# Performance work log

Hardware: AMD Instinct MI355X
Metric: run time of the kernel (lower is better)

## Reference

```python
import jax, jax.numpy as jnp
import numpy as np

B, N, M, D = 8, 4096, 4096, 128


def _cdist(x, y):
    # Euclidean distance via gram trick (matches torch.cdist p=2 math)
    # x: (B,N,D), y: (B,M,D) -> (B,N,M)
    x2 = jnp.sum(x * x, axis=-1)  # (B,N)
    y2 = jnp.sum(y * y, axis=-1)  # (B,M)
    xy = jnp.einsum('bnd,bmd->bnm', x, y)  # (B,N,M)
    sq = x2[:, :, None] + y2[:, None, :] - 2.0 * xy
    return jnp.sqrt(jnp.maximum(sq, 0.0))


def setup_inputs() -> dict:
    key = jax.random.key(0)
    k1, k2 = jax.random.split(key)
    predicted_set = jax.random.normal(k1, (B, N, D), dtype=jnp.float32)
    target_set = jax.random.normal(k2, (B, M, D), dtype=jnp.float32)
    return {"predicted_set": predicted_set, "target_set": target_set}


def reference(predicted_set, target_set):
    pairwise = _cdist(predicted_set, target_set)       # (B,N,M)
    forward_distance = jnp.min(pairwise, axis=1)        # (B,M)  (min over predicted points)
    backward_distance = jnp.min(pairwise, axis=0)       # (N,M)  (min over BATCH, as in original code)
    # reduction = 'mean'
    return jnp.mean(forward_distance) + jnp.mean(backward_distance)
```

## Files before the change

### kernel.cpp

```cpp
#include <hip/hip_runtime.h>
#include <hip/hip_fp8.h>

#define BB 8
#define NN 4096
#define MM 4096
#define DD 128

typedef float f32x4  __attribute__((ext_vector_type(4)));
typedef float f32x16 __attribute__((ext_vector_type(16)));
typedef int   i32x4  __attribute__((ext_vector_type(4)));
typedef int   i32x8  __attribute__((ext_vector_type(8)));


typedef const __attribute__((address_space(1))) unsigned int* gas_ptr;
typedef __attribute__((address_space(3))) unsigned int* las_ptr;
static __device__ __forceinline__ void gload_lds16(const unsigned char* g,
                                                   unsigned char* l) {
    __builtin_amdgcn_global_load_lds((gas_ptr)g, (las_ptr)l, 16, 0, 0);
}

#define ISSUE_X(dst, addr)                                                  \
    asm volatile("global_load_dwordx4 %0, %4, off\n\t"                      \
                 "global_load_dwordx4 %1, %4, off offset:16\n\t"            \
                 "global_load_dwordx4 %2, %4, off offset:2048\n\t"          \
                 "global_load_dwordx4 %3, %4, off offset:2064"              \
                 : "=&v"(dst[0]), "=&v"(dst[1]), "=&v"(dst[2]), "=&v"(dst[3]) \
                 : "v"(addr))

#define WAIT_X(buf, N)                                                      \
    do {                                                                    \
        asm volatile("s_waitcnt vmcnt(" #N ")"                              \
                     : "+v"(buf[0]), "+v"(buf[1]), "+v"(buf[2]), "+v"(buf[3])); \
        __builtin_amdgcn_sched_barrier(0);                                  \
    } while (0)

__global__ __launch_bounds__(256)
void prep_all(const float* __restrict__ x, const float* __restrict__ y,
              unsigned char* __restrict__ xq, unsigned char* __restrict__ yq,
              float* __restrict__ x2, float* __restrict__ y2,
              unsigned int* __restrict__ fwd, float* __restrict__ bsum,
              float* __restrict__ fsum, unsigned int* __restrict__ counter) {
    __shared__ i32x4 lbuf[256];

    const int tid  = threadIdx.x;
    const int g    = blockIdx.x;
    const int gtid = g * 256 + tid;
    if (gtid < BB * MM) fwd[gtid] = 0x7f800000u;
    if (gtid == 0) { *bsum = 0.0f; *fsum = 0.0f; *counter = 0u; }

    const int rl = tid >> 3;
    const int c  = tid & 7;

    const float* src;
    unsigned char* dst;
    float* sq;
    float sgn;
    int row;
    if (g < 1024) {
        src = x; dst = xq + (size_t)g * 4096; sq = x2; sgn = 1.0f;
        row = g * 32 + rl;
    } else {
        src = y; dst = yq + (size_t)(g - 1024) * 4096; sq = y2; sgn = -1.0f;
        row = (g - 1024) * 32 + rl;
    }

    const f32x4* base = (const f32x4*)(src + (size_t)row * DD + c * 16);
    f32x4 v[4];
    #pragma unroll
    for (int j = 0; j < 4; ++j) v[j] = base[j];

    float s = 0.0f;
    #pragma unroll
    for (int j = 0; j < 4; ++j)
        s += v[j].x * v[j].x + v[j].y * v[j].y + v[j].z * v[j].z + v[j].w * v[j].w;

    i32x4 d;
    #pragma unroll
    for (int j = 0; j < 4; ++j) {
        unsigned int dj = (unsigned int)__builtin_amdgcn_cvt_pk_fp8_f32(
            sgn * v[j].x, sgn * v[j].y, 0, false);
        dj = (unsigned int)__builtin_amdgcn_cvt_pk_fp8_f32(
            sgn * v[j].z, sgn * v[j].w, (int)dj, true);
        d[j] = (int)dj;
    }

    const int lds_off = (c >> 2) * 2048 + ((c >> 1) & 1) * 1024
                      + rl * 32 + (c & 1) * 16;
    *(i32x4*)((char*)lbuf + lds_off) = d;

    #pragma unroll
    for (int m = 4; m; m >>= 1) s += __shfl_xor(s, m, 64);
    if (c == 0) sq[row] = 0.5f * s;

    __syncthreads();
    *(i32x4*)(dst + (size_t)tid * 16) = lbuf[tid];
}

__global__ __launch_bounds__(256, 4)
void chamfer_main(const unsigned char* __restrict__ xq, const unsigned char* __restrict__ yq,
                  const float* __restrict__ x2, const float* __restrict__ y2,
                  unsigned int* __restrict__ fwd, float* __restrict__ bpart) {
    __shared__ float x2s[BB][128];
    __shared__ float y2s[BB][32];
    __shared__ unsigned int fbuf[BB][32];
    __shared__ unsigned char ybuf[BB][4096];
    __shared__ float red[4];

    const int tid   = threadIdx.x;
    const int lane  = tid & 63;
    const int wave  = tid >> 6;
    const int lhalf = lane >> 5;
    const int l31   = lane & 31;

    const int id  = blockIdx.x;
    const int xcd = id & 7;
    const int j   = id >> 3;
    const int nb  = (xcd >> 1) * 8 + (j & 7);
    const int mb  = (xcd & 1) * 64 + (j >> 3);
    const int n0b = nb * 128;
    const int n0w = n0b + wave * 32;
    const int m0  = mb * 32;

    const size_t laneoff = (size_t)lhalf * 1024 + (size_t)l31 * 32;
    const unsigned char* xbase = xq + (size_t)(n0w >> 5) * 4096 + laneoff;

    const size_t ysw = (size_t)(wave >> 1) * 2048 + (size_t)(wave & 1) * 1024
                     + ((size_t)lhalf << 4) + (size_t)l31 * 32;
    const unsigned char* ybase = yq + (size_t)mb * 4096 + ysw;

    #pragma unroll
    for (int b = 0; b < BB; ++b)
        gload_lds16(ybase + ((size_t)b << 19), &ybuf[b][wave * 1024]);

    i32x4 fxr[2][4];
    ISSUE_X(fxr[0], xbase);

    for (int i = tid; i < BB * 128; i += 256)
        x2s[i >> 7][i & 127] = x2[(size_t)(i >> 7) * NN + n0b + (i & 127)];
    {
        int i = tid;
        y2s[i >> 5][i & 31] = y2[(size_t)(i >> 5) * MM + m0 + (i & 31)];
        ((unsigned int*)fbuf)[i] = 0x7f800000u;
    }
    __syncthreads();

    const float INF = __builtin_inff();
    float bmin[16];
    #pragma unroll
    for (int r = 0; r < 16; ++r) bmin[r] = INF;

    const int rb0 = lhalf * 1024 + l31 * 16;

    #pragma unroll
    for (int b = 0; b < BB; ++b) {
        const int cur = b & 1;
        if (b < BB - 1)
            ISSUE_X(fxr[cur ^ 1], (xbase + ((size_t)(b + 1) << 19)));

        if (b < BB - 1) { WAIT_X(fxr[cur], 4); }
        else            { WAIT_X(fxr[cur], 0); }

        float y2v = y2s[b][l31];
        f32x16 acc;
        #pragma unroll
        for (int q = 0; q < 4; ++q) {
            f32x4 xv = *(const f32x4*)&x2s[b][wave * 32 + lhalf * 4 + q * 8];
            #pragma unroll
            for (int e = 0; e < 4; ++e)
                acc[q * 4 + e] = xv[e] + y2v;
        }

        #pragma unroll
        for (int i = 0; i < 2; ++i) {
            i32x8 av = __builtin_shufflevector(fxr[cur][2 * i], fxr[cur][2 * i + 1],
                                               0, 1, 2, 3, 4, 5, 6, 7);
            const unsigned char* yb = &ybuf[b][i * 2048 + rb0];
            i32x4 lo = *(const i32x4*)(yb);
            i32x4 hi = *(const i32x4*)(yb + 512);
            i32x8 bv = __builtin_shufflevector(lo, hi, 0, 1, 2, 3, 4, 5, 6, 7);
            acc = __builtin_amdgcn_mfma_scale_f32_32x32x64_f8f6f4(
                av, bv, acc, 0, 0, 0, 127, 0, 127);
        }

        float fm = INF;
        #pragma unroll
        for (int r = 0; r < 16; ++r) {
            bmin[r] = fminf(bmin[r], acc[r]);
            fm      = fminf(fm, acc[r]);
        }
        atomicMin(&fbuf[b][l31], __float_as_uint(fmaxf(fm, 0.0f)));
    }
    __syncthreads();

    {
        int i = tid;
        atomicMin(&fwd[(size_t)(i >> 5) * MM + m0 + (i & 31)], fbuf[i >> 5][i & 31]);
    }

    float s = 0.0f;
    #pragma unroll
    for (int r = 0; r < 16; ++r)
        s += sqrtf(2.0f * fmaxf(bmin[r], 0.0f));
    #pragma unroll
    for (int off = 32; off; off >>= 1) s += __shfl_down(s, off, 64);
    if (lane == 0) red[wave] = s;
    __syncthreads();
    if (tid == 0) bpart[id] = red[0] + red[1] + red[2] + red[3];
}

__global__ __launch_bounds__(256)
void finalize_kernel(const unsigned int* __restrict__ fwd,
                     const float* __restrict__ bpart,
                     float* __restrict__ bsum, float* __restrict__ fsum,
                     unsigned int* __restrict__ counter, float* __restrict__ out) {
    __shared__ float redf[4], redb[4];
    __shared__ int isLast;
    const int tid = threadIdx.x, lane = tid & 63, wave = tid >> 6;
    const int gtid = blockIdx.x * 256 + tid;
    uint4 u = ((const uint4*)fwd)[gtid];
    float sf = sqrtf(2.0f * __uint_as_float(u.x)) + sqrtf(2.0f * __uint_as_float(u.y)) +
               sqrtf(2.0f * __uint_as_float(u.z)) + sqrtf(2.0f * __uint_as_float(u.w));
    float sb = (gtid < 4096) ? bpart[gtid] : 0.0f;
    #pragma unroll
    for (int off = 32; off; off >>= 1) {
        sf += __shfl_down(sf, off, 64);
        sb += __shfl_down(sb, off, 64);
    }
    if (lane == 0) { redf[wave] = sf; redb[wave] = sb; }
    __syncthreads();
    if (tid == 0) {
        atomicAdd(fsum, redf[0] + redf[1] + redf[2] + redf[3]);
        atomicAdd(bsum, redb[0] + redb[1] + redb[2] + redb[3]);
        __threadfence();
        unsigned int c = atomicAdd(counter, 1u);
        isLast = (c == gridDim.x - 1) ? 1 : 0;
        if (isLast) {
            __threadfence();
            float fs = __hip_atomic_load(fsum, __ATOMIC_RELAXED,
                                         __HIP_MEMORY_SCOPE_AGENT);
            float bs = __hip_atomic_load(bsum, __ATOMIC_RELAXED,
                                         __HIP_MEMORY_SCOPE_AGENT);
            out[0] = fs / (float)(BB * MM) + bs / ((float)NN * (float)MM);
        }
    }
}

extern "C" void kernel_launch(void* const* d_in, const int* in_sizes, int n_in,
                              void* d_out, int out_size, void* d_ws, size_t ws_size,
                              hipStream_t stream) {
    const float* x = (const float*)d_in[0];
    const float* y = (const float*)d_in[1];
    float* out = (float*)d_out;

    char* w = (char*)d_ws;
    unsigned char* xq = (unsigned char*)(w);
    unsigned char* yq = (unsigned char*)(w + 4194304);
    float*    x2 = (float*)(w + 8388608);
    float*    y2 = (float*)(w + 8519680);
    unsigned int* fwd = (unsigned int*)(w + 8650752);
    float*    bpart = (float*)(w + 8781824);
    float*    bsum = (float*)(w + 8798208);
    float*    fsum = (float*)(w + 8798212);
    unsigned int* counter = (unsigned int*)(w + 8798216);

    prep_all<<<2048, 256, 0, stream>>>(x, y, xq, yq, x2, y2,
                                       fwd, bsum, fsum, counter);
    chamfer_main<<<4096, 256, 0, stream>>>(xq, yq, x2, y2, fwd, bpart);
    finalize_kernel<<<32, 256, 0, stream>>>(fwd, bpart, bsum, fsum, counter, out);
}
```

Before: 113.4 us.

## Double N-tile per wave in chamfer_main to reuse Y fragments across two MFMAs

```diff
diff --git a/kernel.cpp b/kernel.cpp
--- a/kernel.cpp
+++ b/kernel.cpp
@@ -27,10 +27,11 @@
                  : "=&v"(dst[0]), "=&v"(dst[1]), "=&v"(dst[2]), "=&v"(dst[3]) \
                  : "v"(addr))
 
-#define WAIT_X(buf, N)                                                      \
+#define WAIT_X8(a, c, N)                                                    \
     do {                                                                    \
         asm volatile("s_waitcnt vmcnt(" #N ")"                              \
-                     : "+v"(buf[0]), "+v"(buf[1]), "+v"(buf[2]), "+v"(buf[3])); \
+                     : "+v"(a[0]), "+v"(a[1]), "+v"(a[2]), "+v"(a[3]),      \
+                       "+v"(c[0]), "+v"(c[1]), "+v"(c[2]), "+v"(c[3]));     \
         __builtin_amdgcn_sched_barrier(0);                                  \
     } while (0)
 
@@ -96,11 +97,11 @@
     *(i32x4*)(dst + (size_t)tid * 16) = lbuf[tid];
 }
 
-__global__ __launch_bounds__(256, 4)
+__global__ __launch_bounds__(256, 2)
 void chamfer_main(const unsigned char* __restrict__ xq, const unsigned char* __restrict__ yq,
                   const float* __restrict__ x2, const float* __restrict__ y2,
                   unsigned int* __restrict__ fwd, float* __restrict__ bpart) {
-    __shared__ float x2s[BB][128];
+    __shared__ float x2s[BB][256];
     __shared__ float y2s[BB][32];
     __shared__ unsigned int fbuf[BB][32];
     __shared__ unsigned char ybuf[BB][4096];
@@ -115,10 +116,10 @@
     const int id  = blockIdx.x;
     const int xcd = id & 7;
     const int j   = id >> 3;
-    const int nb  = (xcd >> 1) * 8 + (j & 7);
-    const int mb  = (xcd & 1) * 64 + (j >> 3);
-    const int n0b = nb * 128;
-    const int n0w = n0b + wave * 32;
+    const int nb  = (xcd >> 1) * 4 + (j & 3);
+    const int mb  = (xcd & 1) * 64 + (j >> 2);
+    const int n0b = nb * 256;
+    const int n0w = n0b + wave * 64;
     const int m0  = mb * 32;
 
     const size_t laneoff = (size_t)lhalf * 1024 + (size_t)l31 * 32;
@@ -132,75 +133,91 @@
     for (int b = 0; b < BB; ++b)
         gload_lds16(ybase + ((size_t)b << 19), &ybuf[b][wave * 1024]);
 
-    i32x4 fxr[2][4];
-    ISSUE_X(fxr[0], xbase);
-
-    for (int i = tid; i < BB * 128; i += 256)
-        x2s[i >> 7][i & 127] = x2[(size_t)(i >> 7) * NN + n0b + (i & 127)];
+    i32x4 fxr[2][2][4];
+    ISSUE_X(fxr[0][0], xbase);
+    ISSUE_X(fxr[0][1], (xbase + 4096));
+
+    for (int i = tid; i < BB * 256; i += 256)
+        x2s[i >> 8][i & 255] = x2[(size_t)(i >> 8) * NN + n0b + (i & 255)];
     {
-        int i = tid;
+        int i = tid & 255;
         y2s[i >> 5][i & 31] = y2[(size_t)(i >> 5) * MM + m0 + (i & 31)];
         ((unsigned int*)fbuf)[i] = 0x7f800000u;
     }
     __syncthreads();
 
     const float INF = __builtin_inff();
-    float bmin[16];
-    #pragma unroll
-    for (int r = 0; r < 16; ++r) bmin[r] = INF;
+    float bmin[2][16];
+    #pragma unroll
+    for (int g = 0; g < 2; ++g)
+        #pragma unroll
+        for (int r = 0; r < 16; ++r) bmin[g][r] = INF;
 
     const int rb0 = lhalf * 1024 + l31 * 16;
 
     #pragma unroll
     for (int b = 0; b < BB; ++b) {
         const int cur = b & 1;
-        if (b < BB - 1)
-            ISSUE_X(fxr[cur ^ 1], (xbase + ((size_t)(b + 1) << 19)));
-
-        if (b < BB - 1) { WAIT_X(fxr[cur], 4); }
-        else            { WAIT_X(fxr[cur], 0); }
+        if (b < BB - 1) {
+            const unsigned char* xb = xbase + ((size_t)(b + 1) << 19);
+            ISSUE_X(fxr[cur ^ 1][0], xb);
+            ISSUE_X(fxr[cur ^ 1][1], (xb + 4096));
+        }
+        if (b < BB - 1) { WAIT_X8(fxr[cur][0], fxr[cur][1], 8); }
+        else            { WAIT_X8(fxr[cur][0], fxr[cur][1], 0); }
 
         float y2v = y2s[b][l31];
-        f32x16 acc;
-        #pragma unroll
-        for (int q = 0; q < 4; ++q) {
-            f32x4 xv = *(const f32x4*)&x2s[b][wave * 32 + lhalf * 4 + q * 8];
+        f32x16 acc[2];
+        #pragma unroll
+        for (int g = 0; g < 2; ++g)
             #pragma unroll
-            for (int e = 0; e < 4; ++e)
-                acc[q * 4 + e] = xv[e] + y2v;
-        }
+            for (int q = 0; q < 4; ++q) {
+                f32x4 xv = *(const f32x4*)
+                    &x2s[b][wave * 64 + g * 32 + lhalf * 4 + q * 8];
+                #pragma unroll
+                for (int e = 0; e < 4; ++e)
+                    acc[g][q * 4 + e] = xv[e] + y2v;
+            }
 
         #pragma unroll
         for (int i = 0; i < 2; ++i) {
-            i32x8 av = __builtin_shufflevector(fxr[cur][2 * i], fxr[cur][2 * i + 1],
-                                               0, 1, 2, 3, 4, 5, 6, 7);
             const unsigned char* yb = &ybuf[b][i * 2048 + rb0];
             i32x4 lo = *(const i32x4*)(yb);
             i32x4 hi = *(const i32x4*)(yb + 512);
             i32x8 bv = __builtin_shufflevector(lo, hi, 0, 1, 2, 3, 4, 5, 6, 7);
-            acc = __builtin_amdgcn_mfma_scale_f32_32x32x64_f8f6f4(
-                av, bv, acc, 0, 0, 0, 127, 0, 127);
+            #pragma unroll
+            for (int g = 0; g < 2; ++g) {
+                i32x8 av = __builtin_shufflevector(fxr[cur][g][2 * i],
+                                                   fxr[cur][g][2 * i + 1],
+                                                   0, 1, 2, 3, 4, 5, 6, 7);
+                acc[g] = __builtin_amdgcn_mfma_scale_f32_32x32x64_f8f6f4(
+                    av, bv, acc[g], 0, 0, 0, 127, 0, 127);
+            }
         }
 
         float fm = INF;
         #pragma unroll
-        for (int r = 0; r < 16; ++r) {
-            bmin[r] = fminf(bmin[r], acc[r]);
-            fm      = fminf(fm, acc[r]);
-        }
+        for (int g = 0; g < 2; ++g)
+            #pragma unroll
+            for (int r = 0; r < 16; ++r) {
+                bmin[g][r] = fminf(bmin[g][r], acc[g][r]);
+                fm         = fminf(fm, acc[g][r]);
+            }
         atomicMin(&fbuf[b][l31], __float_as_uint(fmaxf(fm, 0.0f)));
     }
     __syncthreads();
 
     {
-        int i = tid;
+        int i = tid & 255;
         atomicMin(&fwd[(size_t)(i >> 5) * MM + m0 + (i & 31)], fbuf[i >> 5][i & 31]);
     }
 
     float s = 0.0f;
     #pragma unroll
-    for (int r = 0; r < 16; ++r)
-        s += sqrtf(2.0f * fmaxf(bmin[r], 0.0f));
+    for (int g = 0; g < 2; ++g)
+        #pragma unroll
+        for (int r = 0; r < 16; ++r)
+            s += sqrtf(2.0f * fmaxf(bmin[g][r], 0.0f));
     #pragma unroll
     for (int off = 32; off; off >>= 1) s += __shfl_down(s, off, 64);
     if (lane == 0) red[wave] = s;
@@ -220,7 +237,7 @@
     uint4 u = ((const uint4*)fwd)[gtid];
     float sf = sqrtf(2.0f * __uint_as_float(u.x)) + sqrtf(2.0f * __uint_as_float(u.y)) +
                sqrtf(2.0f * __uint_as_float(u.z)) + sqrtf(2.0f * __uint_as_float(u.w));
-    float sb = (gtid < 4096) ? bpart[gtid] : 0.0f;
+    float sb = (gtid < 2048) ? bpart[gtid] : 0.0f;
     #pragma unroll
     for (int off = 32; off; off >>= 1) {
         sf += __shfl_down(sf, off, 64);
@@ -265,6 +282,6 @@
 
     prep_all<<<2048, 256, 0, stream>>>(x, y, xq, yq, x2, y2,
                                        fwd, bsum, fsum, counter);
-    chamfer_main<<<4096, 256, 0, stream>>>(xq, yq, x2, y2, fwd, bpart);
+    chamfer_main<<<2048, 256, 0, stream>>>(xq, yq, x2, y2, fwd, bpart);
     finalize_kernel<<<32, 256, 0, stream>>>(fwd, bpart, bsum, fsum, counter, out);
 }
```

Result: no change. 112.4 us (-0.8%).
